# Performance work log

Hardware: AMD Instinct MI355X
Metric: run time of the kernel (lower is better)

Reference implementation:

```python
import jax, jax.numpy as jnp
import numpy as np

H = 32        # num query heads
KVH = 8       # num kv heads (GQA)
D = 128       # head_size
DV = 128      # head_size_v
SCALE = 0.08838834764831845  # 1/sqrt(128)


def setup_inputs() -> dict:
    key = jax.random.key(0)
    k1, k2, k3 = jax.random.split(key, 3)
    T = 4096  # packed tokens: B=4 sequences of seq_len=1024
    return {
        "query": jax.random.normal(k1, (T, H * D), dtype=jnp.float32),
        "key": jax.random.normal(k2, (T, KVH * D), dtype=jnp.float32),
        "value": jax.random.normal(k3, (T, KVH * DV), dtype=jnp.float32),
        "seq_len": 1024,
    }


def reference(query, key, value, seq_len):
    # Packed varlen causal GQA attention: tokens [T, H*D] split into B
    # sequences of length seq_len, causal mask within each sequence.
    T = query.shape[0]
    B = T // seq_len
    G = H // KVH  # GQA group size

    q = query.reshape(B, seq_len, H, D)
    k = key.reshape(B, seq_len, KVH, D)
    v = value.reshape(B, seq_len, KVH, DV)

    # expand kv heads to match query heads (head i uses kv head i // G)
    k = jnp.repeat(k, G, axis=2)  # [B, S, H, D]
    v = jnp.repeat(v, G, axis=2)  # [B, S, H, DV]

    scores = jnp.einsum("bqhd,bkhd->bhqk", q, k) * SCALE  # [B, H, S, S]
    causal = jnp.tril(jnp.ones((seq_len, seq_len), dtype=bool))
    scores = jnp.where(causal[None, None], scores, jnp.finfo(scores.dtype).min)
    probs = jax.nn.softmax(scores, axis=-1)
    out = jnp.einsum("bhqk,bkhd->bqhd", probs, v)  # [B, S, H, DV]
    return out.reshape(T, H * DV)
```

## Files before the change

kernel.cpp:

```cpp
#include <hip/hip_runtime.h>
#include <hip/hip_bf16.h>

#define H_   32
#define KVH_ 8
#define D_   128
#define DV_  128
#define SEQ_ 1024
#define QKD  (H_*D_)
#define KVD  (KVH_*D_)
#define CS_  (0.08838834764831845f * 1.4426950408889634f)
#define MFIX 8.0f

typedef __attribute__((ext_vector_type(8))) short bf16x8;
typedef __attribute__((ext_vector_type(8))) unsigned short u16x8;
typedef __attribute__((ext_vector_type(4))) float f32x4;
typedef __attribute__((ext_vector_type(4))) unsigned int u32x4;

typedef const __attribute__((address_space(1))) void* gp_t;
typedef __attribute__((address_space(3))) void* lp_t;

#if __has_builtin(__builtin_amdgcn_exp2f)
#define EXP2F(x) __builtin_amdgcn_exp2f(x)
#else
#define EXP2F(x) exp2f(x)
#endif

static __device__ __forceinline__ unsigned short f2b(float x) {
    __hip_bfloat16 b = __float2bfloat16(x);
    return __builtin_bit_cast(unsigned short, b);
}
static __device__ __forceinline__ unsigned pk2(float a, float b) {
    return (unsigned)f2b(a) | ((unsigned)f2b(b) << 16);
}

__global__ __launch_bounds__(256)
void prep_k(const float* __restrict__ K, unsigned short* __restrict__ Kb) {
    const int gt = blockIdx.x * 256 + threadIdx.x;
    const int q  = gt & 15;
    const int r  = gt >> 4;
    const int s  = r & 1023;
    const int bh = r >> 10;
    const int b = bh >> 3, kvh = bh & 7;
    const float* src = K + ((size_t)(b * SEQ_ + s)) * KVD + kvh * D_ + q * 8;
    float4 a = *(const float4*)src;
    float4 c = *(const float4*)(src + 4);
    u32x4 o = { pk2(a.x, a.y), pk2(a.z, a.w), pk2(c.x, c.y), pk2(c.z, c.w) };
    *(u32x4*)(Kb + (size_t)r * 128 + q * 8) = o;
}

__global__ __launch_bounds__(256)
void prep_v(const float* __restrict__ V, unsigned short* __restrict__ Vt) {
    const int gt = blockIdx.x * 256 + threadIdx.x;
    const int dv = gt & 127;
    const int uc = (gt >> 7) & 127;
    const int bh = gt >> 14;
    const int b = bh >> 3, kvh = bh & 7;
    const int C  = uc * 8;
    const int t  = C >> 5;
    const float* src = V + ((size_t)(b * SEQ_)) * KVD + kvh * DV_ + dv;
    unsigned short e[8];
#pragma unroll
    for (int i = 0; i < 8; ++i) {
        const int c = (C + i) & 31;
        const int s = (t << 5) + ((c >> 1) & 15) + ((c & 1) << 4);
        e[i] = f2b(src[(size_t)s * KVD]);
    }
    u16x8 o = { e[0], e[1], e[2], e[3], e[4], e[5], e[6], e[7] };
    *(u16x8*)(Vt + ((size_t)bh * 128 + dv) * SEQ_ + C) = o;
}

__global__ __launch_bounds__(256, 4)
void attn_fwd(const float* __restrict__ Q,
              const unsigned short* __restrict__ Kb,
              const unsigned short* __restrict__ Vt,
              float* __restrict__ O) {
    __shared__ __align__(16) unsigned short KS[2][32 * 128];
    __shared__ __align__(16) unsigned short VT[2][128 * 32];
    __shared__ __align__(16) unsigned int   PW[4][16 * 20];

    const int bid = ((int)blockIdx.x & 7) * 128 + ((int)blockIdx.x >> 3);
    const int p   = bid & 7;
    const int h   = (bid >> 3) & 31;
    const int b   = bid >> 8;
    const int kvh = h >> 2;
    const int bh  = b * 8 + kvh;

    const int tid = threadIdx.x;
    const int w   = tid >> 6;
    const int l   = tid & 63;
    const int lo  = l & 15;
    const int g   = l >> 4;

    const int c0 = w * 128 + l;
    const int c1 = c0 + 64;
    const int kr0 = c0 >> 4, ks0 = c0 & 15;
    const int kr1 = c1 >> 4, ks1 = c1 & 15;
    const int offk0 = kr0 * 256 + (((ks0 & 8) | ((ks0 & 7) ^ (kr0 & 7))) << 4);
    const int offk1 = kr1 * 256 + (((ks1 & 8) | ((ks1 & 7) ^ (kr1 & 7))) << 4);
    const int offv0 = (c0 >> 2) * 2048 + (((c0 & 3) ^ ((c0 >> 3) & 3)) << 4);
    const int offv1 = (c1 >> 2) * 2048 + (((c1 & 3) ^ ((c1 >> 3) & 3)) << 4);

    const char* KbH = (const char*)Kb + (size_t)bh * 262144;
    const char* VtH = (const char*)Vt + (size_t)bh * 262144;
    const char* ksrc0 = KbH + offk0;
    const char* ksrc1 = KbH + offk1;
    const char* vsrc0 = VtH + offv0;
    const char* vsrc1 = VtH + offv1;

    auto issue = [&](int t, int dsel) {
        char* ks = (char*)KS[dsel] + w * 2048;
        char* vs = (char*)VT[dsel] + w * 2048;
        const size_t ko = (size_t)t * 8192;
        const size_t vo = (size_t)t * 64;
        __builtin_amdgcn_global_load_lds((gp_t)(ksrc0 + ko), (lp_t)ks,          16, 0, 0);
        __builtin_amdgcn_global_load_lds((gp_t)(ksrc1 + ko), (lp_t)(ks + 1024), 16, 0, 0);
        __builtin_amdgcn_global_load_lds((gp_t)(vsrc0 + vo), (lp_t)vs,          16, 0, 0);
        __builtin_amdgcn_global_load_lds((gp_t)(vsrc1 + vo), (lp_t)(vs + 1024), 16, 0, 0);
    };

#pragma unroll 1
    for (int ph = 0; ph < 2; ++ph) {
        const int qt     = ph ? (15 - p) : p;
        const int ntiles = 2 * qt + 2;
        const int qw0    = qt * 64 + w * 16;
        const int jmaxw  = (qw0 + 15) >> 5;

        const float* Qb = Q + ((size_t)(b * SEQ_ + qw0 + lo)) * QKD + h * D_;
        bf16x8 qf[4];
#pragma unroll
        for (int cc = 0; cc < 4; ++cc) {
            const float* qp = Qb + cc * 32 + g * 8;
            float4 x0 = *(const float4*)(qp);
            float4 x1 = *(const float4*)(qp + 4);
            bf16x8 f;
            f[0] = f2b(x0.x * CS_); f[1] = f2b(x0.y * CS_);
            f[2] = f2b(x0.z * CS_); f[3] = f2b(x0.w * CS_);
            f[4] = f2b(x1.x * CS_); f[5] = f2b(x1.y * CS_);
            f[6] = f2b(x1.z * CS_); f[7] = f2b(x1.w * CS_);
            qf[cc] = f;
        }

        float lsum[4];
        f32x4 o_[8];
#pragma unroll
        for (int i = 0; i < 4; ++i) lsum[i] = 0.f;
#pragma unroll
        for (int db = 0; db < 8; ++db) o_[db] = (f32x4){0.f, 0.f, 0.f, 0.f};

        __syncthreads();
        issue(0, 0);

        for (int j = 0; j < ntiles; ++j) {
            __syncthreads();
            if (j + 1 < ntiles) issue(j + 1, (j + 1) & 1);
            if (j <= jmaxw) {
                const int k0 = j * 32;
                const int d  = j & 1;

                f32x4 s0 = (f32x4){0.f, 0.f, 0.f, 0.f};
                f32x4 s1 = (f32x4){0.f, 0.f, 0.f, 0.f};
                const int sw = (lo & 7) << 4;
                const char* kbase = (const char*)KS[d];
                __builtin_amdgcn_s_setprio(1);
#pragma unroll
                for (int cc = 0; cc < 4; ++cc) {
                    bf16x8 kf0 = *(const bf16x8*)(kbase + ((lo * 256 + cc * 64 + g * 16) ^ sw));
                    bf16x8 kf1 = *(const bf16x8*)(kbase + (((16 + lo) * 256 + cc * 64 + g * 16) ^ sw));
                    s0 = __builtin_amdgcn_mfma_f32_16x16x32_bf16(qf[cc], kf0, s0, 0, 0, 0);
                    s1 = __builtin_amdgcn_mfma_f32_16x16x32_bf16(qf[cc], kf1, s1, 0, 0, 0);
                }
                __builtin_amdgcn_s_setprio(0);

                const bool needmask = (k0 + 31) > qw0;
#pragma unroll
                for (int i = 0; i < 4; ++i) {
                    float v0 = s0[i], v1 = s1[i];
                    if (needmask) {
                        const int qi = qw0 + 4 * g + i;
                        if (k0 + lo > qi)      v0 = -INFINITY;
                        if (k0 + 16 + lo > qi) v1 = -INFINITY;
                    }
                    const float p0 = EXP2F(v0 - MFIX);
                    const float p1 = EXP2F(v1 - MFIX);
                    lsum[i] += p0 + p1;
                    PW[w][(4 * g + i) * 20 + lo] = pk2(p0, p1);
                }

                bf16x8 pf = *(const bf16x8*)(&PW[w][lo * 20 + g * 4]);
                const char* vbase = (const char*)VT[d];
                const int swv = ((lo >> 1) & 3) << 4;
                __builtin_amdgcn_s_setprio(1);
#pragma unroll
                for (int db = 0; db < 8; ++db) {
                    bf16x8 vf = *(const bf16x8*)(vbase + (db * 16 + lo) * 64 + ((g * 16) ^ swv));
                    o_[db] = __builtin_amdgcn_mfma_f32_16x16x32_bf16(pf, vf, o_[db], 0, 0, 0);
                }
                __builtin_amdgcn_s_setprio(0);
            }
        }

#pragma unroll
        for (int i = 0; i < 4; ++i) {
            float rs = lsum[i];
            rs += __shfl_xor(rs, 1);
            rs += __shfl_xor(rs, 2);
            rs += __shfl_xor(rs, 4);
            rs += __shfl_xor(rs, 8);
            const float inv = 1.0f / rs;
            float* op = O + ((size_t)(b * SEQ_ + qw0 + 4 * g + i)) * (H_ * DV_) + h * DV_ + lo;
#pragma unroll
            for (int db = 0; db < 8; ++db) op[db * 16] = o_[db][i] * inv;
        }
    }
}

extern "C" void kernel_launch(void* const* d_in, const int* in_sizes, int n_in,
                              void* d_out, int out_size, void* d_ws, size_t ws_size,
                              hipStream_t stream) {
    const float* Q = (const float*)d_in[0];
    const float* K = (const float*)d_in[1];
    const float* V = (const float*)d_in[2];
    float* Out = (float*)d_out;
    unsigned short* Kb = (unsigned short*)d_ws;
    unsigned short* Vt = (unsigned short*)((char*)d_ws + 8388608);
    prep_k<<<dim3(2048), dim3(256), 0, stream>>>(K, Kb);
    prep_v<<<dim3(2048), dim3(256), 0, stream>>>(V, Vt);
    attn_fwd<<<dim3(1024), dim3(256), 0, stream>>>(Q, Kb, Vt, Out);
}
```

Before: 80.32 us.

## Compute transposed scores to keep P in registers and merge prep kernels

```diff
diff --git a/kernel.cpp b/kernel.cpp
--- a/kernel.cpp
+++ b/kernel.cpp
@@ -34,39 +34,40 @@
 }
 
 __global__ __launch_bounds__(256)
-void prep_k(const float* __restrict__ K, unsigned short* __restrict__ Kb) {
-    const int gt = blockIdx.x * 256 + threadIdx.x;
-    const int q  = gt & 15;
-    const int r  = gt >> 4;
-    const int s  = r & 1023;
-    const int bh = r >> 10;
-    const int b = bh >> 3, kvh = bh & 7;
-    const float* src = K + ((size_t)(b * SEQ_ + s)) * KVD + kvh * D_ + q * 8;
-    float4 a = *(const float4*)src;
-    float4 c = *(const float4*)(src + 4);
-    u32x4 o = { pk2(a.x, a.y), pk2(a.z, a.w), pk2(c.x, c.y), pk2(c.z, c.w) };
-    *(u32x4*)(Kb + (size_t)r * 128 + q * 8) = o;
-}
-
-__global__ __launch_bounds__(256)
-void prep_v(const float* __restrict__ V, unsigned short* __restrict__ Vt) {
-    const int gt = blockIdx.x * 256 + threadIdx.x;
-    const int dv = gt & 127;
-    const int uc = (gt >> 7) & 127;
-    const int bh = gt >> 14;
-    const int b = bh >> 3, kvh = bh & 7;
-    const int C  = uc * 8;
-    const int t  = C >> 5;
-    const float* src = V + ((size_t)(b * SEQ_)) * KVD + kvh * DV_ + dv;
-    unsigned short e[8];
-#pragma unroll
-    for (int i = 0; i < 8; ++i) {
-        const int c = (C + i) & 31;
-        const int s = (t << 5) + ((c >> 1) & 15) + ((c & 1) << 4);
-        e[i] = f2b(src[(size_t)s * KVD]);
+void prep_kv(const float* __restrict__ K, const float* __restrict__ V,
+             unsigned short* __restrict__ Kb, unsigned short* __restrict__ Vt) {
+    if (blockIdx.x < 2048) {
+        const int gt = blockIdx.x * 256 + threadIdx.x;
+        const int q  = gt & 15;
+        const int r  = gt >> 4;
+        const int s  = r & 1023;
+        const int bh = r >> 10;
+        const int b = bh >> 3, kvh = bh & 7;
+        const float* src = K + ((size_t)(b * SEQ_ + s)) * KVD + kvh * D_ + q * 8;
+        float4 a = *(const float4*)src;
+        float4 c = *(const float4*)(src + 4);
+        u32x4 o = { pk2(a.x, a.y), pk2(a.z, a.w), pk2(c.x, c.y), pk2(c.z, c.w) };
+        *(u32x4*)(Kb + (size_t)r * 128 + q * 8) = o;
+    } else {
+        const int gt = (blockIdx.x - 2048) * 256 + threadIdx.x;
+        const int dv = gt & 127;
+        const int uc = (gt >> 7) & 127;
+        const int bh = gt >> 14;
+        const int b = bh >> 3, kvh = bh & 7;
+        const int C  = uc * 8;
+        const int t  = C >> 5;
+        const float* src = V + ((size_t)(b * SEQ_)) * KVD + kvh * DV_ + dv;
+        unsigned short e[8];
+#pragma unroll
+        for (int i = 0; i < 8; ++i) {
+            const int c = (C & 31) + i;
+            const int kl = 4 * ((c >> 3) & 3) + (c & 3) + 16 * ((c >> 2) & 1);
+            const int s = (t << 5) + kl;
+            e[i] = f2b(src[(size_t)s * KVD]);
+        }
+        u16x8 o = { e[0], e[1], e[2], e[3], e[4], e[5], e[6], e[7] };
+        *(u16x8*)(Vt + ((size_t)bh * 128 + dv) * SEQ_ + C) = o;
     }
-    u16x8 o = { e[0], e[1], e[2], e[3], e[4], e[5], e[6], e[7] };
-    *(u16x8*)(Vt + ((size_t)bh * 128 + dv) * SEQ_ + C) = o;
 }
 
 __global__ __launch_bounds__(256, 4)
@@ -76,7 +77,6 @@
               float* __restrict__ O) {
     __shared__ __align__(16) unsigned short KS[2][32 * 128];
     __shared__ __align__(16) unsigned short VT[2][128 * 32];
-    __shared__ __align__(16) unsigned int   PW[4][16 * 20];
 
     const int bid = ((int)blockIdx.x & 7) * 128 + ((int)blockIdx.x >> 3);
     const int p   = bid & 7;
@@ -140,10 +140,8 @@
             qf[cc] = f;
         }
 
-        float lsum[4];
+        float lsum = 0.f;
         f32x4 o_[8];
-#pragma unroll
-        for (int i = 0; i < 4; ++i) lsum[i] = 0.f;
 #pragma unroll
         for (int db = 0; db < 8; ++db) o_[db] = (f32x4){0.f, 0.f, 0.f, 0.f};
 
@@ -166,27 +164,30 @@
                 for (int cc = 0; cc < 4; ++cc) {
                     bf16x8 kf0 = *(const bf16x8*)(kbase + ((lo * 256 + cc * 64 + g * 16) ^ sw));
                     bf16x8 kf1 = *(const bf16x8*)(kbase + (((16 + lo) * 256 + cc * 64 + g * 16) ^ sw));
-                    s0 = __builtin_amdgcn_mfma_f32_16x16x32_bf16(qf[cc], kf0, s0, 0, 0, 0);
-                    s1 = __builtin_amdgcn_mfma_f32_16x16x32_bf16(qf[cc], kf1, s1, 0, 0, 0);
+                    s0 = __builtin_amdgcn_mfma_f32_16x16x32_bf16(kf0, qf[cc], s0, 0, 0, 0);
+                    s1 = __builtin_amdgcn_mfma_f32_16x16x32_bf16(kf1, qf[cc], s1, 0, 0, 0);
                 }
                 __builtin_amdgcn_s_setprio(0);
 
+                const int q_  = qw0 + lo;
                 const bool needmask = (k0 + 31) > qw0;
+                float pp[8];
 #pragma unroll
                 for (int i = 0; i < 4; ++i) {
                     float v0 = s0[i], v1 = s1[i];
                     if (needmask) {
-                        const int qi = qw0 + 4 * g + i;
-                        if (k0 + lo > qi)      v0 = -INFINITY;
-                        if (k0 + 16 + lo > qi) v1 = -INFINITY;
+                        if (k0 + 4 * g + i > q_)      v0 = -INFINITY;
+                        if (k0 + 16 + 4 * g + i > q_) v1 = -INFINITY;
                     }
-                    const float p0 = EXP2F(v0 - MFIX);
-                    const float p1 = EXP2F(v1 - MFIX);
-                    lsum[i] += p0 + p1;
-                    PW[w][(4 * g + i) * 20 + lo] = pk2(p0, p1);
+                    pp[i]     = EXP2F(v0 - MFIX);
+                    pp[4 + i] = EXP2F(v1 - MFIX);
                 }
-
-                bf16x8 pf = *(const bf16x8*)(&PW[w][lo * 20 + g * 4]);
+                lsum += ((pp[0] + pp[1]) + (pp[2] + pp[3]))
+                      + ((pp[4] + pp[5]) + (pp[6] + pp[7]));
+                u32x4 pu = { pk2(pp[0], pp[1]), pk2(pp[2], pp[3]),
+                             pk2(pp[4], pp[5]), pk2(pp[6], pp[7]) };
+                bf16x8 pf = __builtin_bit_cast(bf16x8, pu);
+
                 const char* vbase = (const char*)VT[d];
                 const int swv = ((lo >> 1) & 3) << 4;
                 __builtin_amdgcn_s_setprio(1);
@@ -199,14 +200,12 @@
             }
         }
 
+        float rs = lsum;
+        rs += __shfl_xor(rs, 16);
+        rs += __shfl_xor(rs, 32);
 #pragma unroll
         for (int i = 0; i < 4; ++i) {
-            float rs = lsum[i];
-            rs += __shfl_xor(rs, 1);
-            rs += __shfl_xor(rs, 2);
-            rs += __shfl_xor(rs, 4);
-            rs += __shfl_xor(rs, 8);
-            const float inv = 1.0f / rs;
+            const float inv = 1.0f / __shfl(rs, 4 * g + i);
             float* op = O + ((size_t)(b * SEQ_ + qw0 + 4 * g + i)) * (H_ * DV_) + h * DV_ + lo;
 #pragma unroll
             for (int db = 0; db < 8; ++db) op[db * 16] = o_[db][i] * inv;
@@ -223,7 +222,6 @@
     float* Out = (float*)d_out;
     unsigned short* Kb = (unsigned short*)d_ws;
     unsigned short* Vt = (unsigned short*)((char*)d_ws + 8388608);
-    prep_k<<<dim3(2048), dim3(256), 0, stream>>>(K, Kb);
-    prep_v<<<dim3(2048), dim3(256), 0, stream>>>(V, Vt);
+    prep_kv<<<dim3(4096), dim3(256), 0, stream>>>(K, V, Kb, Vt);
     attn_fwd<<<dim3(1024), dim3(256), 0, stream>>>(Q, Kb, Vt, Out);
 }
```

New measurement: 72.39 us. -9.9%, faster.
